# Optimization experiments

Hardware: AMD Instinct MI355X
Metric: run time of the kernel (lower is better)

The kernel has to match this reference:

```python
import jax, jax.numpy as jnp
import numpy as np

B, N, C, H, K = 16, 1024, 384, 6, 8
HID = int(C * 2.0)  # mlp_ratio = 2.0
HD = C // H


def _layernorm(x, w, b, eps=1e-5):
    m = x.mean(-1, keepdims=True)
    v = ((x - m) ** 2).mean(-1, keepdims=True)
    return (x - m) * jax.lax.rsqrt(v + eps) * w + b


def setup_inputs() -> dict:
    key = jax.random.key(0)
    ks = jax.random.split(key, 16)
    x = jax.random.normal(ks[0], (B, N, C), jnp.float32)
    # knn indices within each batch, offset by batch*N (as in get_knn_index)
    idx = jax.random.randint(ks[1], (B, K, N), 0, N)
    base = jnp.arange(B, dtype=jnp.int32)[:, None, None] * N
    knn_index = (idx + base).reshape(-1).astype(jnp.int32)
    s = 0.02
    p = {
        "x": x,
        "knn_index": knn_index,
        "ln1_w": jnp.ones((C,), jnp.float32),
        "ln1_b": jnp.zeros((C,), jnp.float32),
        "w_qkv": jax.random.normal(ks[2], (C, 3 * C), jnp.float32) * s,  # qkv_bias=False
        "w_proj": jax.random.normal(ks[3], (C, C), jnp.float32) * s,
        "b_proj": jnp.zeros((C,), jnp.float32),
        "w_knn": jax.random.normal(ks[4], (2 * C, C), jnp.float32) * s,
        "b_knn": jnp.zeros((C,), jnp.float32),
        "w_merge": jax.random.normal(ks[5], (2 * C, C), jnp.float32) * s,
        "b_merge": jnp.zeros((C,), jnp.float32),
        "ln2_w": jnp.ones((C,), jnp.float32),
        "ln2_b": jnp.zeros((C,), jnp.float32),
        "w_fc1": jax.random.normal(ks[6], (C, HID), jnp.float32) * s,
        "b_fc1": jnp.zeros((HID,), jnp.float32),
        "w_fc2": jax.random.normal(ks[7], (HID, C), jnp.float32) * s,
        "b_fc2": jnp.zeros((C,), jnp.float32),
    }
    return p


def reference(x, knn_index, ln1_w, ln1_b, w_qkv, w_proj, b_proj, w_knn, b_knn,
              w_merge, b_merge, ln2_w, ln2_b, w_fc1, b_fc1, w_fc2, b_fc2):
    nx = _layernorm(x, ln1_w, ln1_b)  # [B,N,C]

    # --- self attention ---
    qkv = (nx @ w_qkv).reshape(B, N, 3, H, HD)
    q, k, v = qkv[:, :, 0], qkv[:, :, 1], qkv[:, :, 2]  # [B,N,H,HD]
    scale = HD ** (-0.5)
    attn = jnp.einsum("bnhd,bmhd->bhnm", q, k) * scale
    attn = jax.nn.softmax(attn, axis=-1)
    a_out = jnp.einsum("bhnm,bmhd->bnhd", attn, v).reshape(B, N, C)
    x1 = a_out @ w_proj + b_proj

    # --- graph feature: gather, relative concat, Linear+LeakyReLU, max over k ---
    feat = nx.reshape(B * N, C)[knn_index].reshape(B, K, N, C)
    center = nx[:, None, :, :]  # [B,1,N,C]
    g = jnp.concatenate([feat - center, jnp.broadcast_to(center, (B, K, N, C))], axis=-1)
    knn_f = jax.nn.leaky_relu(g @ w_knn + b_knn, negative_slope=0.2)
    knn_f = knn_f.max(axis=1)  # [B,N,C]

    x1 = jnp.concatenate([x1, knn_f], axis=-1) @ w_merge + b_merge
    x = x + x1

    # --- MLP ---
    h = _layernorm(x, ln2_w, ln2_b)
    h = jax.nn.gelu(h @ w_fc1 + b_fc1, approximate=False) @ w_fc2 + b_fc2
    return x + h
```

## Files before the change

kernel.cpp:

```cpp
#include <hip/hip_runtime.h>
#include <hip/hip_bf16.h>
#include <math.h>

#define BN_ROWS 16384
#define CDIM 384
#define NH 6
#define BBATCH 16
#define NNN 1024

typedef unsigned short u16;
typedef unsigned int u32;
typedef __attribute__((ext_vector_type(8))) short short8;
typedef __attribute__((ext_vector_type(4))) float floatx4;

__device__ __forceinline__ float b2f(u16 s) { return __uint_as_float(((u32)s) << 16); }
__device__ __forceinline__ u16 f2b(float f) {
    __hip_bfloat16 h = __float2bfloat16(f);
    u16 s; __builtin_memcpy(&s, &h, 2); return s;
}
__device__ __forceinline__ void gload_lds16(const u16* g, u16* l) {
    __builtin_amdgcn_global_load_lds(
        (const __attribute__((address_space(1))) unsigned int*)g,
        (__attribute__((address_space(3))) unsigned int*)l, 16, 0, 0);
}

__global__ __launch_bounds__(256) void pack_all(
    const float* __restrict__ W0, u16* __restrict__ T0,
    const float* __restrict__ W1, u16* __restrict__ T1,
    const float* __restrict__ W2, u16* __restrict__ T2,
    const float* __restrict__ W3, u16* __restrict__ T3,
    const float* __restrict__ W4, u16* __restrict__ T4,
    const float* __restrict__ W5, u16* __restrict__ T5)
{
    const float* W; u16* T; int K, N;
    switch (blockIdx.z) {
        case 0: W = W0; T = T0; K = 384; N = 1152; break;
        case 1: W = W1; T = T1; K = 384; N = 384;  break;
        case 2: W = W2; T = T2; K = 768; N = 384;  break;
        case 3: W = W3; T = T3; K = 768; N = 384;  break;
        case 4: W = W4; T = T4; K = 384; N = 768;  break;
        default: W = W5; T = T5; K = 768; N = 384; break;
    }
    const int n0 = blockIdx.x * 32, k0 = blockIdx.y * 32;
    if (n0 >= N || k0 >= K) return;
    __shared__ float s[32][33];
    const int tx = threadIdx.x & 31, ty = threadIdx.x >> 5;
#pragma unroll
    for (int i = 0; i < 4; ++i)
        s[ty + 8 * i][tx] = W[(size_t)(k0 + ty + 8 * i) * N + n0 + tx];
    __syncthreads();
#pragma unroll
    for (int i = 0; i < 4; ++i)
        T[(size_t)(n0 + ty + 8 * i) * K + k0 + tx] = f2b(s[tx][ty + 8 * i]);
}

__global__ __launch_bounds__(64) void ln_kernel(const float* __restrict__ xin,
                                                const float* __restrict__ w,
                                                const float* __restrict__ b,
                                                u16* __restrict__ out)
{
    const int row = blockIdx.x;
    const int t = threadIdx.x;
    const size_t base = (size_t)row * CDIM;
    float v[6];
#pragma unroll
    for (int i = 0; i < 6; ++i) v[i] = xin[base + t + 64 * i];
    float s = 0.f, s2 = 0.f;
#pragma unroll
    for (int i = 0; i < 6; ++i) { s += v[i]; s2 += v[i] * v[i]; }
#pragma unroll
    for (int m = 1; m < 64; m <<= 1) {
        s  += __shfl_xor(s,  m, 64);
        s2 += __shfl_xor(s2, m, 64);
    }
    const float mean = s * (1.0f / CDIM);
    const float var  = s2 * (1.0f / CDIM) - mean * mean;
    const float rs   = rsqrtf(var + 1e-5f);
#pragma unroll
    for (int i = 0; i < 6; ++i) {
        int c = t + 64 * i;
        out[base + c] = f2b((v[i] - mean) * rs * w[c] + b[c]);
    }
}

template<int ACT, bool HAS_BIAS, bool HAS_RES, bool OUT_F32, int MODE, int NT>
__global__ __launch_bounds__(256) void gemm_mfma_kernel(
    const u16* __restrict__ A, int lda,
    const u16* __restrict__ Bt, const u16* __restrict__ Bt2, int ldbt,
    u16* Cb, u16* Cb2, float* Cf, int ldc,
    const float* __restrict__ bias,
    const float* res,
    int K)
{
    constexpr int NTL = NT / 32;
    __shared__ u16 As[2][128 * 32];
    __shared__ u16 Bs[2][NT * 32];
    const int tid  = threadIdx.x;
    const int wv   = tid >> 6;
    const int lane = tid & 63;
    const int l15  = lane & 15;
    const int quad = lane >> 4;
    const int m0 = blockIdx.y * 128;
    const int n0 = blockIdx.x * NT;
    const int woffm = (wv >> 1) * 64;
    const int woffn = (wv & 1) * (NT / 2);

    const u16* bsrc = (MODE == 2 && n0 >= 384) ? Bt2 : Bt;
    const int  bn0  = (MODE == 2 && n0 >= 384) ? (n0 - 384) : n0;

    floatx4 acc[4][NTL];
#pragma unroll
    for (int mt = 0; mt < 4; ++mt)
#pragma unroll
        for (int nt = 0; nt < NTL; ++nt) acc[mt][nt] = (floatx4){0.f, 0.f, 0.f, 0.f};

    const int gsw  = 8 * ((lane & 3) ^ ((lane >> 3) & 3));
    const int rloc = lane >> 2;
    const int rdsw = 8 * (quad ^ ((l15 >> 1) & 3));

    auto stage = [&](int kt, int p) {
#pragma unroll
        for (int j = 0; j < 2; ++j) {
            const int slab = 32 * wv + 16 * j;
            gload_lds16(A + (size_t)(m0 + slab + rloc) * lda + kt + gsw, &As[p][slab * 32]);
        }
        if (NT == 128) {
#pragma unroll
            for (int j = 0; j < 2; ++j) {
                const int slab = 32 * wv + 16 * j;
                gload_lds16(bsrc + (size_t)(bn0 + slab + rloc) * ldbt + kt + gsw, &Bs[p][slab * 32]);
            }
        } else {
            const int slab = 16 * wv;
            gload_lds16(bsrc + (size_t)(bn0 + slab + rloc) * ldbt + kt + gsw, &Bs[p][slab * 32]);
        }
    };

    stage(0, 0);
    __syncthreads();
    int cur = 0;
    for (int kt = 0; kt < K; kt += 32) {
        if (kt + 32 < K) stage(kt + 32, cur ^ 1);

        short8 af[4], bf[NTL];
#pragma unroll
        for (int mt = 0; mt < 4; ++mt)
            af[mt] = *(const short8*)(As[cur] + (woffm + mt * 16 + l15) * 32 + rdsw);
#pragma unroll
        for (int nt = 0; nt < NTL; ++nt)
            bf[nt] = *(const short8*)(Bs[cur] + (woffn + nt * 16 + l15) * 32 + rdsw);
#pragma unroll
        for (int mt = 0; mt < 4; ++mt)
#pragma unroll
            for (int nt = 0; nt < NTL; ++nt)
                acc[mt][nt] = __builtin_amdgcn_mfma_f32_16x16x32_bf16(
                    af[mt], bf[nt], acc[mt][nt], 0, 0, 0);
        __syncthreads();
        cur ^= 1;
    }

#pragma unroll
    for (int nt = 0; nt < NTL; ++nt) {
        const int gc = n0 + woffn + nt * 16 + l15;
        float bi = 0.f;
        if (HAS_BIAS) bi = bias[gc];
        if (MODE == 2) bi = (gc >= 384) ? bias[gc - 384] : 0.f;
#pragma unroll
        for (int mt = 0; mt < 4; ++mt) {
            const int gr0 = m0 + woffm + mt * 16 + quad * 4;
#pragma unroll
            for (int rr = 0; rr < 4; ++rr) {
                float v = acc[mt][nt][rr] + bi;
                if (ACT == 1) v = 0.5f * v * (1.0f + erff(v * 0.70710678118654752f));
                if (HAS_RES)  v += res[(size_t)(gr0 + rr) * ldc + gc];
                if (MODE == 1) {
                    const int t3  = gc / 384;
                    const int rem = gc - t3 * 384;
                    const int hh = rem >> 6, dd = rem & 63;
                    const int bb = (gr0 + rr) >> 10, nn = (gr0 + rr) & 1023;
                    Cb[((size_t)((bb * 6 + hh) * 1024 + nn)) * 192 + t3 * 64 + dd] = f2b(v);
                } else if (MODE == 2) {
                    if (gc < 384) Cb [(size_t)(gr0 + rr) * 384 + gc]       = f2b(v);
                    else          Cb2[(size_t)(gr0 + rr) * 384 + gc - 384] = f2b(v);
                } else if (OUT_F32) {
                    Cf[(size_t)(gr0 + rr) * ldc + gc] = v;
                } else {
                    Cb[(size_t)(gr0 + rr) * ldc + gc] = f2b(v);
                }
            }
        }
    }
}

__global__ __launch_bounds__(256) void attn_mfma_kernel(const u16* __restrict__ qkv2,
                                                        u16* __restrict__ aout)
{
    const int id = blockIdx.x;
    const int rxcd = id & 7;
    const int j = id >> 3;
    const int slab = rxcd + 8 * (j % 12);
    const int qtile = j / 12;
    const int b = slab / NH, h = slab % NH;

    const int wave = threadIdx.x >> 6;
    const int lane = threadIdx.x & 63;
    const int l15 = lane & 15;
    const int quad = lane >> 4;
    const int qbase = qtile * 128 + wave * 32;
    const int tid = threadIdx.x;

    const u16* slabp = qkv2 + ((size_t)(b * NH + h) << 10) * 192;

    __shared__ __align__(16) u16 Ks[64 * 72];
    __shared__ __align__(16) u16 Vt[64 * 72];
    __shared__ __align__(16) u16 Ps[4][32 * 72];
    __shared__ __align__(16) float Ls[4][32];

    short8 qf[2][2];
#pragma unroll
    for (int nt = 0; nt < 2; ++nt) {
        const u16* qrow = slabp + (size_t)(qbase + nt * 16 + l15) * 192;
        qf[nt][0] = *(const short8*)(qrow + quad * 8);
        qf[nt][1] = *(const short8*)(qrow + 32 + quad * 8);
    }

    float rowsum[2] = {0.f, 0.f};
    floatx4 Oacc[2][4];
#pragma unroll
    for (int mt = 0; mt < 2; ++mt)
#pragma unroll
        for (int nt = 0; nt < 4; ++nt) Oacc[mt][nt] = (floatx4){0.f, 0.f, 0.f, 0.f};

    for (int kc = 0; kc < NNN; kc += 64) {
        {
            const int key = tid >> 2, dblk = (tid & 3) * 16;
            const u16* kp = slabp + (size_t)(kc + key) * 192 + 64 + dblk;
            *(short8*)(Ks + key * 72 + dblk)     = *(const short8*)(kp);
            *(short8*)(Ks + key * 72 + dblk + 8) = *(const short8*)(kp + 8);
        }
        {
            const int kp2 = tid & 31, db = (tid >> 5) * 8;
            const u16* v0p = slabp + (size_t)(kc + 2 * kp2) * 192 + 128 + db;
            uint4 v0 = *(const uint4*)(v0p);
            uint4 v1 = *(const uint4*)(v0p + 192);
            u32 a0[4] = {v0.x, v0.y, v0.z, v0.w};
            u32 a1[4] = {v1.x, v1.y, v1.z, v1.w};
#pragma unroll
            for (int i = 0; i < 8; ++i) {
                u32 w0 = (i & 1) ? (a0[i >> 1] >> 16) : (a0[i >> 1] & 0xffffu);
                u32 w1 = (i & 1) ? (a1[i >> 1] >> 16) : (a1[i >> 1] & 0xffffu);
                *(u32*)(Vt + (size_t)(db + i) * 72 + 2 * kp2) = w0 | (w1 << 16);
            }
        }
        __syncthreads();

        floatx4 sc[4][2];
#pragma unroll
        for (int kt_ = 0; kt_ < 4; ++kt_) {
            short8 kf0 = *(const short8*)(Ks + (kt_ * 16 + l15) * 72 + quad * 8);
            short8 kf1 = *(const short8*)(Ks + (kt_ * 16 + l15) * 72 + 32 + quad * 8);
#pragma unroll
            for (int nt = 0; nt < 2; ++nt) {
                floatx4 s = {0.f, 0.f, 0.f, 0.f};
                s = __builtin_amdgcn_mfma_f32_16x16x32_bf16(kf0, qf[nt][0], s, 0, 0, 0);
                s = __builtin_amdgcn_mfma_f32_16x16x32_bf16(kf1, qf[nt][1], s, 0, 0, 0);
                sc[kt_][nt] = s;
            }
        }

#pragma unroll
        for (int kt_ = 0; kt_ < 4; ++kt_)
#pragma unroll
            for (int nt = 0; nt < 2; ++nt) {
                u16 pk[4];
#pragma unroll
                for (int rr = 0; rr < 4; ++rr) {
                    float p = __expf(sc[kt_][nt][rr] * 0.125f);
                    rowsum[nt] += p;
                    pk[rr] = f2b(p);
                }
                u32 lo = (u32)pk[0] | ((u32)pk[1] << 16);
                u32 hi = (u32)pk[2] | ((u32)pk[3] << 16);
                *(uint2*)(Ps[wave] + (nt * 16 + l15) * 72 + kt_ * 16 + quad * 4) =
                    make_uint2(lo, hi);
            }

        short8 pf[2][2];
#pragma unroll
        for (int mt = 0; mt < 2; ++mt) {
            pf[mt][0] = *(const short8*)(Ps[wave] + (mt * 16 + l15) * 72 + quad * 8);
            pf[mt][1] = *(const short8*)(Ps[wave] + (mt * 16 + l15) * 72 + 32 + quad * 8);
        }
#pragma unroll
        for (int nt = 0; nt < 4; ++nt) {
#pragma unroll
            for (int kk = 0; kk < 2; ++kk) {
                short8 vf = *(const short8*)(Vt + (size_t)(nt * 16 + l15) * 72 + kk * 32 + quad * 8);
#pragma unroll
                for (int mt = 0; mt < 2; ++mt)
                    Oacc[mt][nt] = __builtin_amdgcn_mfma_f32_16x16x32_bf16(
                        pf[mt][kk], vf, Oacc[mt][nt], 0, 0, 0);
            }
        }
        __syncthreads();
    }

#pragma unroll
    for (int nt = 0; nt < 2; ++nt) {
        float l = rowsum[nt];
        l += __shfl_xor(l, 16, 64);
        l += __shfl_xor(l, 32, 64);
        if (quad == 0) Ls[wave][nt * 16 + l15] = l;
    }
#pragma unroll
    for (int mt = 0; mt < 2; ++mt) {
        float4 lv = *(const float4*)&Ls[wave][mt * 16 + quad * 4];
        float li[4] = {lv.x, lv.y, lv.z, lv.w};
#pragma unroll
        for (int rr = 0; rr < 4; ++rr) {
            float inv = 1.0f / li[rr];
            int q = qbase + mt * 16 + quad * 4 + rr;
#pragma unroll
            for (int nt = 0; nt < 4; ++nt)
                aout[(size_t)(b * NNN + q) * CDIM + h * 64 + nt * 16 + l15] =
                    f2b(Oacc[mt][nt][rr] * inv);
        }
    }
}

__global__ __launch_bounds__(128) void knnmax_kernel(const u16* __restrict__ t1,
                                                     const u16* __restrict__ t2,
                                                     const int* __restrict__ idx,
                                                     u16* __restrict__ x1cat)
{
    const int bn = blockIdx.x * 2 + (threadIdx.x >> 6);
    const int lane = threadIdx.x & 63;
    if (lane >= 48) return;
    const int b = bn >> 10, n = bn & 1023;
    int ind[8];
#pragma unroll
    for (int k = 0; k < 8; ++k) ind[k] = idx[b * 8192 + k * 1024 + n];
    const int c0 = lane * 8;
    const size_t rbase = (size_t)bn * CDIM + c0;
    short8 v1 = *(const short8*)(t1 + rbase);
    short8 v2 = *(const short8*)(t2 + rbase);
    float basef[8], mx[8];
#pragma unroll
    for (int j = 0; j < 8; ++j) {
        basef[j] = b2f((u16)v2[j]) - b2f((u16)v1[j]);
        mx[j] = -1e30f;
    }
#pragma unroll
    for (int k = 0; k < 8; ++k) {
        short8 nv = *(const short8*)(t1 + (size_t)ind[k] * CDIM + c0);
#pragma unroll
        for (int j = 0; j < 8; ++j) {
            float v = b2f((u16)nv[j]) + basef[j];
            v = (v > 0.f) ? v : 0.2f * v;
            mx[j] = fmaxf(mx[j], v);
        }
    }
    short8 ov;
#pragma unroll
    for (int j = 0; j < 8; ++j) ov[j] = (short)f2b(mx[j]);
    *(short8*)(x1cat + (size_t)bn * 768 + CDIM + c0) = ov;
}

extern "C" void kernel_launch(void* const* d_in, const int* in_sizes, int n_in,
                              void* d_out, int out_size, void* d_ws, size_t ws_size,
                              hipStream_t stream)
{
    (void)in_sizes; (void)n_in; (void)out_size; (void)ws_size;
    const float* x     = (const float*)d_in[0];
    const int*   knn   = (const int*)d_in[1];
    const float* ln1w  = (const float*)d_in[2];
    const float* ln1b  = (const float*)d_in[3];
    const float* wqkv  = (const float*)d_in[4];
    const float* wproj = (const float*)d_in[5];
    const float* bproj = (const float*)d_in[6];
    const float* wknn  = (const float*)d_in[7];
    const float* bknn  = (const float*)d_in[8];
    const float* wmrg  = (const float*)d_in[9];
    const float* bmrg  = (const float*)d_in[10];
    const float* ln2w  = (const float*)d_in[11];
    const float* ln2b  = (const float*)d_in[12];
    const float* wfc1  = (const float*)d_in[13];
    const float* bfc1  = (const float*)d_in[14];
    const float* wfc2  = (const float*)d_in[15];
    const float* bfc2  = (const float*)d_in[16];

    u16* wsb = (u16*)d_ws;
    const size_t RE = (size_t)BN_ROWS * CDIM;
    u16* nxb   = wsb;
    u16* qkvb  = wsb + RE;
    u16* x1cat = wsb + RE;
    u16* t1b   = wsb + 3 * RE;
    u16* hinb  = wsb;
    u16* h1b   = wsb + RE;
    u16* wqkvT  = wsb + 4 * RE;
    u16* wprojT = wqkvT + 442368;
    u16* wknnT  = wprojT + 147456;
    u16* wmrgT  = wknnT + 294912;
    u16* wfc1T  = wmrgT + 294912;
    u16* wfc2T  = wfc1T + 294912;
    u16*   aoutb = (u16*)d_out;
    u16*   t2b   = (u16*)d_out;
    float* xmid  = (float*)d_out;

    pack_all<<<dim3(36, 24, 6), 256, 0, stream>>>(
        wqkv, wqkvT, wproj, wprojT, wknn, wknnT, wmrg, wmrgT, wfc1, wfc1T, wfc2, wfc2T);
    ln_kernel<<<BN_ROWS, 64, 0, stream>>>(x, ln1w, ln1b, nxb);
    gemm_mfma_kernel<0, false, false, false, 1, 128><<<dim3(9, 128), 256, 0, stream>>>(
        nxb, CDIM, wqkvT, nullptr, CDIM, qkvb, nullptr, nullptr, 0, nullptr, nullptr, CDIM);
    attn_mfma_kernel<<<768, 256, 0, stream>>>(qkvb, aoutb);
    gemm_mfma_kernel<0, true, false, false, 0, 64><<<dim3(6, 128), 256, 0, stream>>>(
        aoutb, CDIM, wprojT, nullptr, CDIM, x1cat, nullptr, nullptr, 768, bproj, nullptr, CDIM);
    gemm_mfma_kernel<0, false, false, false, 2, 128><<<dim3(6, 128), 256, 0, stream>>>(
        nxb, CDIM, wknnT, wknnT + 384, 768, t1b, t2b, nullptr, CDIM, bknn, nullptr, CDIM);
    knnmax_kernel<<<BN_ROWS / 2, 128, 0, stream>>>(t1b, t2b, knn, x1cat);
    gemm_mfma_kernel<0, true, true, true, 0, 64><<<dim3(6, 128), 256, 0, stream>>>(
        x1cat, 768, wmrgT, nullptr, 768, nullptr, nullptr, xmid, CDIM, bmrg, x, 768);
    ln_kernel<<<BN_ROWS, 64, 0, stream>>>(xmid, ln2w, ln2b, hinb);
    gemm_mfma_kernel<1, true, false, false, 0, 128><<<dim3(6, 128), 256, 0, stream>>>(
        hinb, CDIM, wfc1T, nullptr, CDIM, h1b, nullptr, nullptr, 768, bfc1, nullptr, CDIM);
    gemm_mfma_kernel<0, true, true, true, 0, 64><<<dim3(6, 128), 256, 0, stream>>>(
        h1b, 768, wfc2T, nullptr, 768, nullptr, nullptr, (float*)d_out, CDIM, bfc2, xmid, 768);
}
```

Measured before the change: 346.8 us.

## Swizzle GEMM block order, use packed bf16 cvt, perm-based V transpose, MFMA priority

The GEMM kernel remaps the linear block index so that consecutive blocks are spread across 8 groups, which may change L2 locality across XCDs. The attention kernel now converts softmax probabilities with the hardware packed bf16 instruction instead of scalar conversions. It builds the V transpose with byte-permute instructions instead of shifts and masks. It also raises wave priority around the MFMA sections. These are separate instruction-level and scheduling tweaks. The swizzle assumes the total block count is divisible by 8, and the inline asm conversion may round differently from the old helper.

New measurement: 318.0 us. 1.09x faster.

```diff
diff --git a/kernel.cpp b/kernel.cpp
--- a/kernel.cpp
+++ b/kernel.cpp
@@ -17,6 +17,11 @@
 __device__ __forceinline__ u16 f2b(float f) {
     __hip_bfloat16 h = __float2bfloat16(f);
     u16 s; __builtin_memcpy(&s, &h, 2); return s;
+}
+__device__ __forceinline__ u32 cvt_pk_bf16(float lo, float hi) {
+    u32 r;
+    asm("v_cvt_pk_bf16_f32 %0, %1, %2" : "=v"(r) : "v"(lo), "v"(hi));
+    return r;
 }
 __device__ __forceinline__ void gload_lds16(const u16* g, u16* l) {
     __builtin_amdgcn_global_load_lds(
@@ -100,8 +105,15 @@
     const int lane = tid & 63;
     const int l15  = lane & 15;
     const int quad = lane >> 4;
-    const int m0 = blockIdx.y * 128;
-    const int n0 = blockIdx.x * NT;
+
+    const int nbx = gridDim.x;
+    const int total = nbx * gridDim.y;
+    int lin = blockIdx.x + nbx * blockIdx.y;
+    const int cpx = total >> 3;
+    lin = (lin & 7) * cpx + (lin >> 3);
+    const int m0 = (lin / nbx) * 128;
+    const int n0 = (lin % nbx) * NT;
+
     const int woffm = (wv >> 1) * 64;
     const int woffn = (wv & 1) * (NT / 2);
 
@@ -246,15 +258,17 @@
             u32 a0[4] = {v0.x, v0.y, v0.z, v0.w};
             u32 a1[4] = {v1.x, v1.y, v1.z, v1.w};
 #pragma unroll
-            for (int i = 0; i < 8; ++i) {
-                u32 w0 = (i & 1) ? (a0[i >> 1] >> 16) : (a0[i >> 1] & 0xffffu);
-                u32 w1 = (i & 1) ? (a1[i >> 1] >> 16) : (a1[i >> 1] & 0xffffu);
-                *(u32*)(Vt + (size_t)(db + i) * 72 + 2 * kp2) = w0 | (w1 << 16);
+            for (int i = 0; i < 4; ++i) {
+                u32 lo = __builtin_amdgcn_perm(a1[i], a0[i], 0x05040100u);
+                u32 hi = __builtin_amdgcn_perm(a1[i], a0[i], 0x07060302u);
+                *(u32*)(Vt + (size_t)(db + 2 * i)     * 72 + 2 * kp2) = lo;
+                *(u32*)(Vt + (size_t)(db + 2 * i + 1) * 72 + 2 * kp2) = hi;
             }
         }
         __syncthreads();
 
         floatx4 sc[4][2];
+        __builtin_amdgcn_s_setprio(1);
 #pragma unroll
         for (int kt_ = 0; kt_ < 4; ++kt_) {
             short8 kf0 = *(const short8*)(Ks + (kt_ * 16 + l15) * 72 + quad * 8);
@@ -267,20 +281,20 @@
                 sc[kt_][nt] = s;
             }
         }
+        __builtin_amdgcn_s_setprio(0);
 
 #pragma unroll
         for (int kt_ = 0; kt_ < 4; ++kt_)
 #pragma unroll
             for (int nt = 0; nt < 2; ++nt) {
-                u16 pk[4];
+                float pv[4];
 #pragma unroll
                 for (int rr = 0; rr < 4; ++rr) {
-                    float p = __expf(sc[kt_][nt][rr] * 0.125f);
-                    rowsum[nt] += p;
-                    pk[rr] = f2b(p);
+                    pv[rr] = __expf(sc[kt_][nt][rr] * 0.125f);
+                    rowsum[nt] += pv[rr];
                 }
-                u32 lo = (u32)pk[0] | ((u32)pk[1] << 16);
-                u32 hi = (u32)pk[2] | ((u32)pk[3] << 16);
+                u32 lo = cvt_pk_bf16(pv[0], pv[1]);
+                u32 hi = cvt_pk_bf16(pv[2], pv[3]);
                 *(uint2*)(Ps[wave] + (nt * 16 + l15) * 72 + kt_ * 16 + quad * 4) =
                     make_uint2(lo, hi);
             }
@@ -291,6 +305,7 @@
             pf[mt][0] = *(const short8*)(Ps[wave] + (mt * 16 + l15) * 72 + quad * 8);
             pf[mt][1] = *(const short8*)(Ps[wave] + (mt * 16 + l15) * 72 + 32 + quad * 8);
         }
+        __builtin_amdgcn_s_setprio(1);
 #pragma unroll
         for (int nt = 0; nt < 4; ++nt) {
 #pragma unroll
@@ -302,6 +317,7 @@
                         pf[mt][kk], vf, Oacc[mt][nt], 0, 0, 0);
             }
         }
+        __builtin_amdgcn_s_setprio(0);
         __syncthreads();
     }
 
```
